# Optimization experiments

Hardware: AMD Instinct MI355X
Metric: run time of the kernel (lower is better)

Reference implementation:

```python
import jax, jax.numpy as jnp
import numpy as np

NUM_CLASSES = 80
IGNORE = 0.5
LABEL_SMOOTH = 0.0
MAX_GT = 20
C = 5 + NUM_CLASSES
SIZES = (13, 26, 52)
BS = 64
ANCHORS = jnp.array([
    [[0.0240, 0.0313], [0.0385, 0.0721], [0.0793, 0.0553]],
    [[0.0721, 0.1466], [0.1490, 0.1082], [0.1418, 0.2861]],
    [[0.2788, 0.2163], [0.3750, 0.4760], [0.8966, 0.7837]],
], dtype=jnp.float32)
ANCH_REV = ANCHORS[::-1]  # anchors[[2,1,0]] in the torch code


def bce(p, t):
    p = jnp.clip(p, 1e-7, 1.0 - 1e-7)
    return -t * jnp.log(p) - (1.0 - t) * jnp.log(1.0 - p)


def cal_iou(b1, b2):
    tl = jnp.maximum(b1[..., 0:2] - b1[..., 2:4] / 2, b2[..., 0:2] - b2[..., 2:4] / 2)
    br = jnp.minimum(b1[..., 0:2] + b1[..., 2:4] / 2, b2[..., 0:2] + b2[..., 2:4] / 2)
    wh = jnp.maximum(br - tl, 0.0)
    inter = wh[..., 0] * wh[..., 1]
    union = b1[..., 2] * b1[..., 3] + b2[..., 2] * b2[..., 3] - inter
    return inter / jnp.clip(union, 1e-6)


def _sample_loss(preds, tflat):
    # preds: [N, C] decoded (x,y,w,h,conf,cls...); tflat: [M, C] target grid flattened
    N = preds.shape[0]
    conf_t = tflat[:, 4]
    _, idx = jax.lax.top_k(conf_t, MAX_GT)      # gather up to MAX_GT GT slots
    gts = tflat[idx]                            # [K, C]
    gmask = gts[:, 4]                           # 1.0 for real GT, 0.0 for padding
    iou = cal_iou(gts[:, None, :4], preds[None, :, :4])  # [K, N]
    best = jnp.argmax(iou, axis=-1)             # [K]
    sel = preds[best]                           # [K, C]
    reg = jnp.sum((sel[:, :4] - gts[:, :4]) ** 2, axis=-1) * (2.0 - gts[:, 2] * gts[:, 3])
    loss_reg = jnp.sum(gmask * reg)
    tar_cls = gts[:, 5:] * (1.0 - LABEL_SMOOTH) + LABEL_SMOOTH / NUM_CLASSES
    loss_cls = jnp.sum(gmask[:, None] * bce(sel[:, 5:], tar_cls))
    # noobj mask: zero at best-matched preds (valid GTs only) and at high-IoU preds
    noobj = jnp.ones(N, preds.dtype).at[best].multiply(1.0 - gmask)
    maxiou = jnp.max(iou * gmask[:, None], axis=0)  # [N]
    noobj = noobj * (maxiou < IGNORE).astype(preds.dtype)
    loss_conf = jnp.sum(gmask * bce(sel[:, 4], 1.0)) + jnp.sum(noobj * bce(preds[:, 4], 0.0))
    return loss_reg + loss_conf + loss_cls


def _scale_loss(pred, tgt, l):
    bs, lsz = pred.shape[0], pred.shape[-1]
    p = pred.reshape(bs, 3, C, lsz, lsz).transpose(0, 1, 3, 4, 2)  # [bs,3,h,w,C]
    raw_w, raw_h = p[..., 2], p[..., 3]
    s = jax.nn.sigmoid(p)
    grid = jnp.arange(lsz, dtype=p.dtype)
    x = (grid[None, None, None, :] + s[..., 0]) / lsz
    y = (grid[None, None, :, None] + s[..., 1]) / lsz
    anch = ANCH_REV[l]  # [3,2]
    w = anch[:, 0][None, :, None, None] * jnp.exp(raw_w)
    h = anch[:, 1][None, :, None, None] * jnp.exp(raw_h)
    boxes = jnp.stack([x, y, w, h], axis=-1)
    preds = jnp.concatenate([boxes, s[..., 4:5], s[..., 5:]], axis=-1).reshape(bs, -1, C)
    tflat = tgt.reshape(bs, -1, C)
    return jnp.sum(jax.vmap(_sample_loss)(preds, tflat))


def setup_inputs() -> dict:
    key = jax.random.key(0)
    ks = jax.random.split(key, 6)
    inp = {}
    for i, lsz in enumerate(SIZES):
        inp['pred%d' % i] = jax.random.normal(ks[i], (BS, 3 * C, lsz, lsz), dtype=jnp.float32)
        M = 3 * lsz * lsz
        kb, ki, kc = jax.random.split(ks[3 + i], 3)
        xywh = jax.random.uniform(kb, (BS, MAX_GT, 4), minval=0.05, maxval=0.6, dtype=jnp.float32)
        cls_idx = jax.random.randint(kc, (BS, MAX_GT), 0, NUM_CLASSES)
        entry = jnp.concatenate([xywh, jnp.ones((BS, MAX_GT, 1), jnp.float32),
                                 jax.nn.one_hot(cls_idx, NUM_CLASSES, dtype=jnp.float32)], axis=-1)
        pos = jax.random.randint(ki, (BS, MAX_GT), 0, M)
        tflat = jnp.zeros((BS, M, C), jnp.float32).at[jnp.arange(BS)[:, None], pos].set(entry)
        inp['targets%d' % i] = tflat.reshape(BS, 3, lsz, lsz, C)
    return inp


def reference(pred0, pred1, pred2, targets0, targets1, targets2):
    return (_scale_loss(pred0, targets0, 0)
            + _scale_loss(pred1, targets1, 1)
            + _scale_loss(pred2, targets2, 2))
```

## Files before the change

### kernel.cpp

```cpp
#include <hip/hip_runtime.h>

#define CC 85
#define NC 80
#define MAXGT 20
#define BSZ 64
#define IGNORE_T 0.5f
#define CHUNK 1024

#define N0 507
#define N1 2028
#define N2 8112
#define R0 (BSZ*N0)
#define R1 (BSZ*N1)
#define R2 (BSZ*N2)
#define RTOT (R0+R1+R2)

#define POS_B   (192u*MAXGT*4u)
#define KEYS_B  (192u*MAXGT*8u)
#define NOOBJ_B (192u*4u)
#define HDR_B   (POS_B + KEYS_B + NOOBJ_B + 192u*4u)
#define BOX_B   ((unsigned)RTOT*16u)

__constant__ float d_anch[3][3][2] = {
  {{0.2788f,0.2163f},{0.375f,0.476f},{0.8966f,0.7837f}},
  {{0.0721f,0.1466f},{0.149f,0.1082f},{0.1418f,0.2861f}},
  {{0.024f,0.0313f},{0.0385f,0.0721f},{0.0793f,0.0553f}},
};
__constant__ int d_lsz[3] = {13,26,52};

__device__ __forceinline__ float sigmoidf(float x){ return 1.0f/(1.0f+__expf(-x)); }
__device__ __forceinline__ float bcef(float p, float t){
  p = fminf(fmaxf(p, 1e-7f), 1.0f-1e-7f);
  return -t*__logf(p) - (1.0f-t)*__logf(1.0f-p);
}
__device__ __forceinline__ float iouf(float gx,float gy,float gw,float gh,
                                      float px,float py,float pw,float ph){
  float tlx = fmaxf(gx-gw*0.5f, px-pw*0.5f);
  float tly = fmaxf(gy-gh*0.5f, py-ph*0.5f);
  float brx = fminf(gx+gw*0.5f, px+pw*0.5f);
  float bry = fminf(gy+gh*0.5f, py+ph*0.5f);
  float w = fmaxf(brx-tlx, 0.0f), h = fmaxf(bry-tly, 0.0f);
  float inter = w*h;
  float uni = gw*gh + pw*ph - inter;
  return inter / fmaxf(uni, 1e-6f);
}

template<int LSZ>
__device__ __forceinline__ void scanbox_one(const float* __restrict__ tgt,
                                            const float* __restrict__ pred,
                                            int rl, int s, int gofs,
                                            int* __restrict__ ws_pos,
                                            int* __restrict__ ws_cnt,
                                            float4* __restrict__ box4,
                                            float* __restrict__ confr){
  const int L2 = LSZ*LSZ, N = 3*L2;
  int b = rl / N;
  int n = rl - b*N;
  float c = tgt[(size_t)rl*CC + 4];
  if(c > 0.5f){
    int slot = s*BSZ + b;
    int i = atomicAdd(&ws_cnt[slot], 1);
    if(i < MAXGT) ws_pos[slot*MAXGT + i] = n;
  }
  int a = n / L2, rem = n - a*L2;
  int ii = rem / LSZ, jj = rem - ii*LSZ;
  const float* base = pred + (size_t)b*3*CC*L2 + (size_t)a*CC*L2 + rem;
  float q0 = base[0];
  float q1 = base[L2];
  float q2 = base[2*L2];
  float q3 = base[3*L2];
  float q4 = base[4*L2];
  const float inv = 1.0f/(float)LSZ;
  float px = ((float)jj + sigmoidf(q0))*inv;
  float py = ((float)ii + sigmoidf(q1))*inv;
  float pw = d_anch[s][a][0]*__expf(q2);
  float ph = d_anch[s][a][1]*__expf(q3);
  box4[gofs + rl] = make_float4(px,py,pw,ph);
  confr[gofs + rl] = q4;
}

__global__ __launch_bounds__(256)
void k_scanbox(const float* __restrict__ t0, const float* __restrict__ t1,
               const float* __restrict__ t2,
               const float* __restrict__ p0, const float* __restrict__ p1,
               const float* __restrict__ p2,
               int* __restrict__ ws_pos, int* __restrict__ ws_cnt,
               float4* __restrict__ box4, float* __restrict__ confr){
  int r = blockIdx.x*256 + threadIdx.x;
  if(r < R0)         scanbox_one<13>(t0, p0, r,       0, 0,     ws_pos, ws_cnt, box4, confr);
  else if(r < R0+R1) scanbox_one<26>(t1, p1, r-R0,    1, R0,    ws_pos, ws_cnt, box4, confr);
  else if(r < RTOT)  scanbox_one<52>(t2, p2, r-R0-R1, 2, R0+R1, ws_pos, ws_cnt, box4, confr);
}

__global__ __launch_bounds__(256, 2)
void k_iou(const float* __restrict__ t0, const float* __restrict__ t1,
           const float* __restrict__ t2,
           const float4* __restrict__ box4, const float* __restrict__ confr,
           const int* __restrict__ ws_pos, const int* __restrict__ ws_cnt,
           unsigned long long* __restrict__ ws_keys,
           float* __restrict__ ws_noobj){
  int s = blockIdx.z, b = blockIdx.y;
  int lsz = d_lsz[s], lsz2 = lsz*lsz, N = 3*lsz2;
  int n0 = blockIdx.x*CHUNK;
  if(n0 >= N) return;
  int slot = s*BSZ + b;
  int gofs = (s==0 ? 0 : (s==1 ? R0 : R0+R1)) + b*N;
  const float* tgt = (s==0 ? t0 : (s==1 ? t1 : t2)) + (size_t)b*N*CC;
  const float4* bx = box4 + gofs;
  const float*  cf = confr + gofs;
  int tid = threadIdx.x;
  __shared__ float gx[MAXGT], gy[MAXGT], gw[MAXGT], gh[MAXGT];
  __shared__ unsigned long long lkey[4][MAXGT];
  __shared__ float lnob[4];
  if(tid < MAXGT){
    int G = ws_cnt[slot];
    float x=0.f,y=0.f,w=0.f,h=0.f;
    if(tid < G){
      const float* r = tgt + (size_t)ws_pos[slot*MAXGT+tid]*CC;
      x=r[0]; y=r[1]; w=r[2]; h=r[3];
    }
    gx[tid]=x; gy[tid]=y; gw[tid]=w; gh[tid]=h;
  }
  __syncthreads();
  unsigned long long key[MAXGT];
  #pragma unroll
  for(int g=0; g<MAXGT; g++) key[g] = 0ull;
  float noobj = 0.0f;
  int nend = min(n0+CHUNK, N);
  for(int n=n0+tid; n<nend; n+=256){
    float4 B = bx[n];
    float q4 = cf[n];
    float maxiou = 0.0f;
    unsigned int ninv = ~(unsigned int)n;
    #pragma unroll
    for(int g=0; g<MAXGT; g++){
      float io = iouf(gx[g],gy[g],gw[g],gh[g], B.x,B.y,B.z,B.w);
      maxiou = fmaxf(maxiou, io);
      unsigned long long k = ((unsigned long long)__float_as_uint(io) << 32) | (unsigned long long)ninv;
      key[g] = (k > key[g]) ? k : key[g];
    }
    if(maxiou < IGNORE_T) noobj += bcef(sigmoidf(q4), 0.0f);
  }
  int wid = tid >> 6, lane = tid & 63;
  #pragma unroll
  for(int g=0; g<MAXGT; g++){
    unsigned long long k = key[g];
    for(int off=32; off>0; off>>=1){
      unsigned long long o = __shfl_down(k, off, 64);
      k = (o > k) ? o : k;
    }
    if(lane == 0) lkey[wid][g] = k;
  }
  for(int off=32; off>0; off>>=1) noobj += __shfl_down(noobj, off, 64);
  if(lane == 0) lnob[wid] = noobj;
  __syncthreads();
  if(tid < MAXGT){
    unsigned long long k0 = lkey[0][tid] > lkey[1][tid] ? lkey[0][tid] : lkey[1][tid];
    unsigned long long k1 = lkey[2][tid] > lkey[3][tid] ? lkey[2][tid] : lkey[3][tid];
    unsigned long long k  = k0 > k1 ? k0 : k1;
    atomicMax(&ws_keys[slot*MAXGT+tid], k);
  }
  if(tid == 0) atomicAdd(&ws_noobj[slot], lnob[0]+lnob[1]+lnob[2]+lnob[3]);
}

__global__ __launch_bounds__(256)
void k_final(const float* __restrict__ p0, const float* __restrict__ p1,
             const float* __restrict__ p2,
             const float* __restrict__ t0, const float* __restrict__ t1,
             const float* __restrict__ t2,
             const int* __restrict__ ws_pos, const int* __restrict__ ws_cnt,
             const unsigned long long* __restrict__ ws_keys,
             const float* __restrict__ ws_noobj,
             float* __restrict__ out){
  int b = blockIdx.x, s = blockIdx.y, z = blockIdx.z;
  int lsz = d_lsz[s], lsz2 = lsz*lsz, N = 3*lsz2;
  int slot = s*BSZ + b;
  const float* pred = (s==0 ? p0 : (s==1 ? p1 : p2)) + (size_t)b*3*CC*lsz2;
  const float* tgt  = (s==0 ? t0 : (s==1 ? t1 : t2)) + (size_t)b*N*CC;
  int tid = threadIdx.x;
  __shared__ int bn[MAXGT];
  __shared__ int gp[MAXGT];
  __shared__ float sx[MAXGT], sy[MAXGT], sw[MAXGT], sh[MAXGT];
  int G = ws_cnt[slot];
  if(tid < MAXGT){
    unsigned long long k = ws_keys[slot*MAXGT + tid];
    bn[tid] = (int)(~(unsigned int)(k & 0xffffffffull));
    float x=0.f,y=0.f,w=0.f,h=0.f; int p=0;
    if(tid < G){
      p = ws_pos[slot*MAXGT + tid];
      const float* r = tgt + (size_t)p*CC;
      x=r[0]; y=r[1]; w=r[2]; h=r[3];
    }
    gp[tid]=p; sx[tid]=x; sy[tid]=y; sw[tid]=w; sh[tid]=h;
  }
  __syncthreads();
  float loss = 0.0f;
  float inv = 1.0f/(float)lsz;
  if(z == 0 && tid < G){
    int n = bn[tid];
    int a = n/lsz2, rem = n - a*lsz2, i = rem/lsz, j = rem - i*lsz;
    const float* base = pred + (size_t)a*CC*lsz2 + rem;
    float q0 = base[0];
    float q1 = base[(size_t)lsz2];
    float q2 = base[2*(size_t)lsz2];
    float q3 = base[3*(size_t)lsz2];
    float q4 = base[4*(size_t)lsz2];
    float px = ((float)j + sigmoidf(q0))*inv;
    float py = ((float)i + sigmoidf(q1))*inv;
    float pw = d_anch[s][a][0]*__expf(q2);
    float ph = d_anch[s][a][1]*__expf(q3);
    float dx=px-sx[tid], dy=py-sy[tid], dw=pw-sw[tid], dh=ph-sh[tid];
    loss += (dx*dx + dy*dy + dw*dw + dh*dh) * (2.0f - sw[tid]*sh[tid]);
    loss += bcef(sigmoidf(q4), 1.0f);
    bool first = true;
    for(int g2=0; g2<tid; g2++) if(bn[g2]==n) first=false;
    if(first){
      float maxiou = 0.0f;
      for(int g2=0; g2<MAXGT; g2++)
        maxiou = fmaxf(maxiou, iouf(sx[g2],sy[g2],sw[g2],sh[g2], px,py,pw,ph));
      if(maxiou < IGNORE_T) loss -= bcef(sigmoidf(q4), 0.0f);
    }
  }
  for(int idx = z*256 + tid; idx < G*NC; idx += 1024){
    int g = idx/NC, c = idx - g*NC;
    int n = bn[g];
    int a = n/lsz2, rem = n - a*lsz2;
    float q = pred[(size_t)a*CC*lsz2 + (size_t)(5+c)*lsz2 + rem];
    float tcls = tgt[(size_t)gp[g]*CC + 5 + c];
    loss += bcef(sigmoidf(q), tcls);
  }
  if(z == 0 && tid == 0) loss += ws_noobj[slot];
  __shared__ float wsum[4];
  for(int off=32; off>0; off>>=1) loss += __shfl_down(loss, off, 64);
  if((tid & 63) == 0) wsum[tid>>6] = loss;
  __syncthreads();
  if(tid==0){
    float v = wsum[0]+wsum[1]+wsum[2]+wsum[3];
    if(v != 0.0f || z == 0) atomicAdd(out, v);
  }
}

extern "C" void kernel_launch(void* const* d_in, const int* in_sizes, int n_in,
                              void* d_out, int out_size, void* d_ws, size_t ws_size,
                              hipStream_t stream) {
  const float* p0 = (const float*)d_in[0];
  const float* t0 = (const float*)d_in[1];
  const float* p1 = (const float*)d_in[2];
  const float* t1 = (const float*)d_in[3];
  const float* p2 = (const float*)d_in[4];
  const float* t2 = (const float*)d_in[5];
  float* out = (float*)d_out;
  char* ws = (char*)d_ws;
  int*                ws_pos   = (int*)(ws);
  unsigned long long* ws_keys  = (unsigned long long*)(ws + POS_B);
  float*              ws_noobj = (float*)(ws + POS_B + KEYS_B);
  int*                ws_cnt   = (int*)(ws + POS_B + KEYS_B + NOOBJ_B);
  float4*             ws_box4  = (float4*)(ws + HDR_B);
  float*              ws_confr = (float*)(ws + HDR_B + BOX_B);

  hipMemsetAsync(ws, 0, HDR_B, stream);
  hipMemsetAsync(d_out, 0, sizeof(float), stream);

  k_scanbox<<<(RTOT+255)/256, 256, 0, stream>>>(t0,t1,t2, p0,p1,p2,
                                                ws_pos, ws_cnt, ws_box4, ws_confr);
  k_iou    <<<dim3(8,BSZ,3), 256, 0, stream>>>(t0,t1,t2, ws_box4, ws_confr,
                                               ws_pos, ws_cnt, ws_keys, ws_noobj);
  k_final  <<<dim3(BSZ,3,4), 256, 0, stream>>>(p0,p1,p2, t0,t1,t2,
                                               ws_pos, ws_cnt, ws_keys, ws_noobj, out);
}
```

Baseline: 412.8 us.

## Fuse scan, IoU and final loss into one block-per-sample kernel

Replaces the three-kernel pipeline (scan/box decode, chunked IoU, final loss) plus memsets with a single kernel that gives each (scale, batch) sample its own 512-thread block. That block finds the GT slots, decodes boxes in registers, computes IoU with GT corners and areas precomputed, and finishes the loss. A small second kernel then sums the per-slot results, which removes global atomics and the workspace round-trips for boxes. The risk is reduced parallelism: only 192 blocks run, and the 52x52 scale blocks each process 8112 cells serially, which may leave load imbalance and idle CUs.

New measurement: 421.0 us. Within noise of the previous version (+2.0%).

```diff
diff --git a/kernel.cpp b/kernel.cpp
--- a/kernel.cpp
+++ b/kernel.cpp
@@ -5,266 +5,225 @@
 #define MAXGT 20
 #define BSZ 64
 #define IGNORE_T 0.5f
-#define CHUNK 1024
-
-#define N0 507
-#define N1 2028
-#define N2 8112
-#define R0 (BSZ*N0)
-#define R1 (BSZ*N1)
-#define R2 (BSZ*N2)
-#define RTOT (R0+R1+R2)
-
-#define POS_B   (192u*MAXGT*4u)
-#define KEYS_B  (192u*MAXGT*8u)
-#define NOOBJ_B (192u*4u)
-#define HDR_B   (POS_B + KEYS_B + NOOBJ_B + 192u*4u)
-#define BOX_B   ((unsigned)RTOT*16u)
+#define BT 512
+#define NWAVE (BT/64)
 
 __constant__ float d_anch[3][3][2] = {
   {{0.2788f,0.2163f},{0.375f,0.476f},{0.8966f,0.7837f}},
   {{0.0721f,0.1466f},{0.149f,0.1082f},{0.1418f,0.2861f}},
   {{0.024f,0.0313f},{0.0385f,0.0721f},{0.0793f,0.0553f}},
 };
-__constant__ int d_lsz[3] = {13,26,52};
 
 __device__ __forceinline__ float sigmoidf(float x){ return 1.0f/(1.0f+__expf(-x)); }
 __device__ __forceinline__ float bcef(float p, float t){
   p = fminf(fmaxf(p, 1e-7f), 1.0f-1e-7f);
   return -t*__logf(p) - (1.0f-t)*__logf(1.0f-p);
 }
-__device__ __forceinline__ float iouf(float gx,float gy,float gw,float gh,
-                                      float px,float py,float pw,float ph){
-  float tlx = fmaxf(gx-gw*0.5f, px-pw*0.5f);
-  float tly = fmaxf(gy-gh*0.5f, py-ph*0.5f);
-  float brx = fminf(gx+gw*0.5f, px+pw*0.5f);
-  float bry = fminf(gy+gh*0.5f, py+ph*0.5f);
-  float w = fmaxf(brx-tlx, 0.0f), h = fmaxf(bry-tly, 0.0f);
-  float inter = w*h;
-  float uni = gw*gh + pw*ph - inter;
-  return inter / fmaxf(uni, 1e-6f);
-}
-
-template<int LSZ>
-__device__ __forceinline__ void scanbox_one(const float* __restrict__ tgt,
-                                            const float* __restrict__ pred,
-                                            int rl, int s, int gofs,
-                                            int* __restrict__ ws_pos,
-                                            int* __restrict__ ws_cnt,
-                                            float4* __restrict__ box4,
-                                            float* __restrict__ confr){
-  const int L2 = LSZ*LSZ, N = 3*L2;
-  int b = rl / N;
-  int n = rl - b*N;
-  float c = tgt[(size_t)rl*CC + 4];
-  if(c > 0.5f){
-    int slot = s*BSZ + b;
-    int i = atomicAdd(&ws_cnt[slot], 1);
-    if(i < MAXGT) ws_pos[slot*MAXGT + i] = n;
-  }
-  int a = n / L2, rem = n - a*L2;
-  int ii = rem / LSZ, jj = rem - ii*LSZ;
-  const float* base = pred + (size_t)b*3*CC*L2 + (size_t)a*CC*L2 + rem;
-  float q0 = base[0];
-  float q1 = base[L2];
-  float q2 = base[2*L2];
-  float q3 = base[3*L2];
-  float q4 = base[4*L2];
-  const float inv = 1.0f/(float)LSZ;
-  float px = ((float)jj + sigmoidf(q0))*inv;
-  float py = ((float)ii + sigmoidf(q1))*inv;
-  float pw = d_anch[s][a][0]*__expf(q2);
-  float ph = d_anch[s][a][1]*__expf(q3);
-  box4[gofs + rl] = make_float4(px,py,pw,ph);
-  confr[gofs + rl] = q4;
-}
-
-__global__ __launch_bounds__(256)
-void k_scanbox(const float* __restrict__ t0, const float* __restrict__ t1,
-               const float* __restrict__ t2,
-               const float* __restrict__ p0, const float* __restrict__ p1,
-               const float* __restrict__ p2,
-               int* __restrict__ ws_pos, int* __restrict__ ws_cnt,
-               float4* __restrict__ box4, float* __restrict__ confr){
-  int r = blockIdx.x*256 + threadIdx.x;
-  if(r < R0)         scanbox_one<13>(t0, p0, r,       0, 0,     ws_pos, ws_cnt, box4, confr);
-  else if(r < R0+R1) scanbox_one<26>(t1, p1, r-R0,    1, R0,    ws_pos, ws_cnt, box4, confr);
-  else if(r < RTOT)  scanbox_one<52>(t2, p2, r-R0-R1, 2, R0+R1, ws_pos, ws_cnt, box4, confr);
-}
-
-__global__ __launch_bounds__(256, 2)
-void k_iou(const float* __restrict__ t0, const float* __restrict__ t1,
-           const float* __restrict__ t2,
-           const float4* __restrict__ box4, const float* __restrict__ confr,
-           const int* __restrict__ ws_pos, const int* __restrict__ ws_cnt,
-           unsigned long long* __restrict__ ws_keys,
-           float* __restrict__ ws_noobj){
-  int s = blockIdx.z, b = blockIdx.y;
-  int lsz = d_lsz[s], lsz2 = lsz*lsz, N = 3*lsz2;
-  int n0 = blockIdx.x*CHUNK;
-  if(n0 >= N) return;
-  int slot = s*BSZ + b;
-  int gofs = (s==0 ? 0 : (s==1 ? R0 : R0+R1)) + b*N;
-  const float* tgt = (s==0 ? t0 : (s==1 ? t1 : t2)) + (size_t)b*N*CC;
-  const float4* bx = box4 + gofs;
-  const float*  cf = confr + gofs;
-  int tid = threadIdx.x;
-  __shared__ float gx[MAXGT], gy[MAXGT], gw[MAXGT], gh[MAXGT];
-  __shared__ unsigned long long lkey[4][MAXGT];
-  __shared__ float lnob[4];
-  if(tid < MAXGT){
-    int G = ws_cnt[slot];
+
+struct SlotSmem {
+  int cnt;
+  int pos[MAXGT];
+  int bn[MAXGT];
+  float gx[MAXGT], gy[MAXGT], gw[MAXGT], gh[MAXGT];
+  float4 tb[MAXGT];
+  float area[MAXGT];
+  unsigned long long lkey[NWAVE][MAXGT];
+  float lnob[NWAVE];
+  float lloss[NWAVE];
+};
+
+template<int LSZ, int S>
+__device__ __forceinline__ void slot_loss(const float* __restrict__ pred,
+                                          const float* __restrict__ tgt,
+                                          float* __restrict__ out_slot,
+                                          SlotSmem& sm)
+{
+  constexpr int L2 = LSZ*LSZ;
+  constexpr int N  = 3*L2;
+  const int tid = threadIdx.x;
+
+  if (tid == 0) sm.cnt = 0;
+  __syncthreads();
+  for (int n = tid; n < N; n += BT) {
+    if (tgt[(size_t)n*CC + 4] > 0.5f) {
+      int i = atomicAdd(&sm.cnt, 1);
+      if (i < MAXGT) sm.pos[i] = n;
+    }
+  }
+  __syncthreads();
+  const int G = min(sm.cnt, MAXGT);
+
+  if (tid < MAXGT) {
     float x=0.f,y=0.f,w=0.f,h=0.f;
-    if(tid < G){
-      const float* r = tgt + (size_t)ws_pos[slot*MAXGT+tid]*CC;
+    if (tid < G) {
+      const float* r = tgt + (size_t)sm.pos[tid]*CC;
       x=r[0]; y=r[1]; w=r[2]; h=r[3];
     }
-    gx[tid]=x; gy[tid]=y; gw[tid]=w; gh[tid]=h;
-  }
-  __syncthreads();
+    sm.gx[tid]=x; sm.gy[tid]=y; sm.gw[tid]=w; sm.gh[tid]=h;
+    sm.tb[tid] = make_float4(x-w*0.5f, y-h*0.5f, x+w*0.5f, y+h*0.5f);
+    sm.area[tid] = w*h;
+  }
+  __syncthreads();
+
   unsigned long long key[MAXGT];
   #pragma unroll
-  for(int g=0; g<MAXGT; g++) key[g] = 0ull;
+  for (int g=0; g<MAXGT; g++) key[g]=0ull;
   float noobj = 0.0f;
-  int nend = min(n0+CHUNK, N);
-  for(int n=n0+tid; n<nend; n+=256){
-    float4 B = bx[n];
-    float q4 = cf[n];
-    float maxiou = 0.0f;
-    unsigned int ninv = ~(unsigned int)n;
-    #pragma unroll
-    for(int g=0; g<MAXGT; g++){
-      float io = iouf(gx[g],gy[g],gw[g],gh[g], B.x,B.y,B.z,B.w);
-      maxiou = fmaxf(maxiou, io);
-      unsigned long long k = ((unsigned long long)__float_as_uint(io) << 32) | (unsigned long long)ninv;
-      key[g] = (k > key[g]) ? k : key[g];
-    }
-    if(maxiou < IGNORE_T) noobj += bcef(sigmoidf(q4), 0.0f);
-  }
-  int wid = tid >> 6, lane = tid & 63;
+  const float inv = 1.0f/(float)LSZ;
+
+  for (int base = 0; base < N; base += BT*4) {
+    float rx0[4],rx1[4],ry0[4],ry1[4],pa[4],q4v[4],maxi[4];
+    int nr[4];
+    #pragma unroll
+    for (int r=0;r<4;r++){
+      const int n = base + r*BT + tid;
+      nr[r]=n; maxi[r]=0.f;
+      if (n < N) {
+        const int a = n/L2, rem = n - a*L2;
+        const int ii = rem/LSZ, jj = rem - ii*LSZ;
+        const float* bp = pred + (size_t)a*CC*L2 + rem;
+        const float q0=bp[0], q1=bp[L2], q2=bp[2*L2], q3=bp[3*L2];
+        q4v[r]=bp[4*L2];
+        const float px = ((float)jj + sigmoidf(q0))*inv;
+        const float py = ((float)ii + sigmoidf(q1))*inv;
+        const float pw = d_anch[S][a][0]*__expf(q2);
+        const float ph = d_anch[S][a][1]*__expf(q3);
+        rx0[r]=px-pw*0.5f; rx1[r]=px+pw*0.5f;
+        ry0[r]=py-ph*0.5f; ry1[r]=py+ph*0.5f;
+        pa[r]=pw*ph;
+      } else {
+        rx0[r]=0.f; rx1[r]=0.f; ry0[r]=0.f; ry1[r]=0.f; pa[r]=0.f; q4v[r]=0.f;
+      }
+    }
+    #pragma unroll
+    for (int g=0; g<MAXGT; g++){
+      const float4 tb = sm.tb[g];
+      const float ga = sm.area[g];
+      #pragma unroll
+      for (int r=0;r<4;r++){
+        const float w = fmaxf(fminf(tb.z,rx1[r]) - fmaxf(tb.x,rx0[r]), 0.0f);
+        const float h = fmaxf(fminf(tb.w,ry1[r]) - fmaxf(tb.y,ry0[r]), 0.0f);
+        const float inter = w*h;
+        const float io = inter / fmaxf(ga + pa[r] - inter, 1e-6f);
+        maxi[r] = fmaxf(maxi[r], io);
+        const unsigned long long k =
+          ((unsigned long long)__float_as_uint(io)<<32) |
+          (unsigned long long)(~(unsigned)nr[r]);
+        if (k > key[g]) key[g] = k;
+      }
+    }
+    #pragma unroll
+    for (int r=0;r<4;r++)
+      if (nr[r] < N && maxi[r] < IGNORE_T) noobj += bcef(sigmoidf(q4v[r]), 0.0f);
+  }
+
+  const int wid = tid>>6, lane = tid&63;
   #pragma unroll
-  for(int g=0; g<MAXGT; g++){
+  for (int g=0; g<MAXGT; g++){
     unsigned long long k = key[g];
-    for(int off=32; off>0; off>>=1){
-      unsigned long long o = __shfl_down(k, off, 64);
-      k = (o > k) ? o : k;
-    }
-    if(lane == 0) lkey[wid][g] = k;
-  }
-  for(int off=32; off>0; off>>=1) noobj += __shfl_down(noobj, off, 64);
-  if(lane == 0) lnob[wid] = noobj;
-  __syncthreads();
-  if(tid < MAXGT){
-    unsigned long long k0 = lkey[0][tid] > lkey[1][tid] ? lkey[0][tid] : lkey[1][tid];
-    unsigned long long k1 = lkey[2][tid] > lkey[3][tid] ? lkey[2][tid] : lkey[3][tid];
-    unsigned long long k  = k0 > k1 ? k0 : k1;
-    atomicMax(&ws_keys[slot*MAXGT+tid], k);
-  }
-  if(tid == 0) atomicAdd(&ws_noobj[slot], lnob[0]+lnob[1]+lnob[2]+lnob[3]);
-}
-
-__global__ __launch_bounds__(256)
-void k_final(const float* __restrict__ p0, const float* __restrict__ p1,
-             const float* __restrict__ p2,
-             const float* __restrict__ t0, const float* __restrict__ t1,
-             const float* __restrict__ t2,
-             const int* __restrict__ ws_pos, const int* __restrict__ ws_cnt,
-             const unsigned long long* __restrict__ ws_keys,
-             const float* __restrict__ ws_noobj,
-             float* __restrict__ out){
-  int b = blockIdx.x, s = blockIdx.y, z = blockIdx.z;
-  int lsz = d_lsz[s], lsz2 = lsz*lsz, N = 3*lsz2;
-  int slot = s*BSZ + b;
-  const float* pred = (s==0 ? p0 : (s==1 ? p1 : p2)) + (size_t)b*3*CC*lsz2;
-  const float* tgt  = (s==0 ? t0 : (s==1 ? t1 : t2)) + (size_t)b*N*CC;
-  int tid = threadIdx.x;
-  __shared__ int bn[MAXGT];
-  __shared__ int gp[MAXGT];
-  __shared__ float sx[MAXGT], sy[MAXGT], sw[MAXGT], sh[MAXGT];
-  int G = ws_cnt[slot];
-  if(tid < MAXGT){
-    unsigned long long k = ws_keys[slot*MAXGT + tid];
-    bn[tid] = (int)(~(unsigned int)(k & 0xffffffffull));
-    float x=0.f,y=0.f,w=0.f,h=0.f; int p=0;
-    if(tid < G){
-      p = ws_pos[slot*MAXGT + tid];
-      const float* r = tgt + (size_t)p*CC;
-      x=r[0]; y=r[1]; w=r[2]; h=r[3];
-    }
-    gp[tid]=p; sx[tid]=x; sy[tid]=y; sw[tid]=w; sh[tid]=h;
-  }
-  __syncthreads();
+    for (int off=32; off>0; off>>=1){
+      const unsigned long long o = __shfl_down(k, off, 64);
+      if (o > k) k = o;
+    }
+    if (lane==0) sm.lkey[wid][g] = k;
+  }
+  for (int off=32; off>0; off>>=1) noobj += __shfl_down(noobj, off, 64);
+  if (lane==0) sm.lnob[wid] = noobj;
+  __syncthreads();
+  if (tid < MAXGT){
+    unsigned long long k = sm.lkey[0][tid];
+    #pragma unroll
+    for (int w=1; w<NWAVE; w++){ const unsigned long long o = sm.lkey[w][tid]; if (o>k) k=o; }
+    sm.bn[tid] = (int)(~(unsigned)(k & 0xffffffffull));
+  }
+  __syncthreads();
+
   float loss = 0.0f;
-  float inv = 1.0f/(float)lsz;
-  if(z == 0 && tid < G){
-    int n = bn[tid];
-    int a = n/lsz2, rem = n - a*lsz2, i = rem/lsz, j = rem - i*lsz;
-    const float* base = pred + (size_t)a*CC*lsz2 + rem;
-    float q0 = base[0];
-    float q1 = base[(size_t)lsz2];
-    float q2 = base[2*(size_t)lsz2];
-    float q3 = base[3*(size_t)lsz2];
-    float q4 = base[4*(size_t)lsz2];
-    float px = ((float)j + sigmoidf(q0))*inv;
-    float py = ((float)i + sigmoidf(q1))*inv;
-    float pw = d_anch[s][a][0]*__expf(q2);
-    float ph = d_anch[s][a][1]*__expf(q3);
-    float dx=px-sx[tid], dy=py-sy[tid], dw=pw-sw[tid], dh=ph-sh[tid];
-    loss += (dx*dx + dy*dy + dw*dw + dh*dh) * (2.0f - sw[tid]*sh[tid]);
+  if (tid < G){
+    const int n = sm.bn[tid];
+    const int a = n/L2, rem = n - a*L2, i = rem/LSZ, j = rem - i*LSZ;
+    const float* bp = pred + (size_t)a*CC*L2 + rem;
+    const float q0=bp[0], q1=bp[L2], q2=bp[2*L2], q3=bp[3*L2], q4=bp[4*L2];
+    const float px = ((float)j + sigmoidf(q0))*inv;
+    const float py = ((float)i + sigmoidf(q1))*inv;
+    const float pw = d_anch[S][a][0]*__expf(q2);
+    const float ph = d_anch[S][a][1]*__expf(q3);
+    const float dx=px-sm.gx[tid], dy=py-sm.gy[tid], dw=pw-sm.gw[tid], dh=ph-sm.gh[tid];
+    loss += (dx*dx+dy*dy+dw*dw+dh*dh)*(2.0f - sm.gw[tid]*sm.gh[tid]);
     loss += bcef(sigmoidf(q4), 1.0f);
     bool first = true;
-    for(int g2=0; g2<tid; g2++) if(bn[g2]==n) first=false;
-    if(first){
+    for (int g2=0; g2<tid; g2++) if (sm.bn[g2]==n) first=false;
+    if (first){
       float maxiou = 0.0f;
-      for(int g2=0; g2<MAXGT; g2++)
-        maxiou = fmaxf(maxiou, iouf(sx[g2],sy[g2],sw[g2],sh[g2], px,py,pw,ph));
-      if(maxiou < IGNORE_T) loss -= bcef(sigmoidf(q4), 0.0f);
-    }
-  }
-  for(int idx = z*256 + tid; idx < G*NC; idx += 1024){
-    int g = idx/NC, c = idx - g*NC;
-    int n = bn[g];
-    int a = n/lsz2, rem = n - a*lsz2;
-    float q = pred[(size_t)a*CC*lsz2 + (size_t)(5+c)*lsz2 + rem];
-    float tcls = tgt[(size_t)gp[g]*CC + 5 + c];
-    loss += bcef(sigmoidf(q), tcls);
-  }
-  if(z == 0 && tid == 0) loss += ws_noobj[slot];
-  __shared__ float wsum[4];
-  for(int off=32; off>0; off>>=1) loss += __shfl_down(loss, off, 64);
-  if((tid & 63) == 0) wsum[tid>>6] = loss;
-  __syncthreads();
-  if(tid==0){
-    float v = wsum[0]+wsum[1]+wsum[2]+wsum[3];
-    if(v != 0.0f || z == 0) atomicAdd(out, v);
-  }
+      const float bx0=px-pw*0.5f, bx1=px+pw*0.5f, by0=py-ph*0.5f, by1=py+ph*0.5f;
+      const float parea=pw*ph;
+      for (int g2=0; g2<MAXGT; g2++){
+        const float4 tb = sm.tb[g2];
+        const float w = fmaxf(fminf(tb.z,bx1) - fmaxf(tb.x,bx0), 0.0f);
+        const float h = fmaxf(fminf(tb.w,by1) - fmaxf(tb.y,by0), 0.0f);
+        const float inter = w*h;
+        maxiou = fmaxf(maxiou, inter / fmaxf(sm.area[g2]+parea-inter, 1e-6f));
+      }
+      if (maxiou < IGNORE_T) loss -= bcef(sigmoidf(q4), 0.0f);
+    }
+  }
+  for (int idx = tid; idx < G*NC; idx += BT){
+    const int g = idx/NC, c = idx - g*NC;
+    const int n = sm.bn[g];
+    const int a = n/L2, rem = n - a*L2;
+    const float q  = pred[(size_t)a*CC*L2 + (size_t)(5+c)*L2 + rem];
+    const float tc = tgt[(size_t)sm.pos[g]*CC + 5 + c];
+    loss += bcef(sigmoidf(q), tc);
+  }
+  for (int off=32; off>0; off>>=1) loss += __shfl_down(loss, off, 64);
+  if (lane==0) sm.lloss[wid] = loss;
+  __syncthreads();
+  if (tid==0){
+    float v = 0.f;
+    #pragma unroll
+    for (int w=0; w<NWAVE; w++) v += sm.lloss[w] + sm.lnob[w];
+    *out_slot = v;
+  }
+}
+
+__global__ __launch_bounds__(BT, 2)
+void k_fused(const float* __restrict__ p0, const float* __restrict__ t0,
+             const float* __restrict__ p1, const float* __restrict__ t1,
+             const float* __restrict__ p2, const float* __restrict__ t2,
+             float* __restrict__ slot_out)
+{
+  __shared__ SlotSmem sm;
+  const int b = blockIdx.x, s = blockIdx.y;
+  float* o = slot_out + s*BSZ + b;
+  if (s==0)      slot_loss<13,0>(p0 + (size_t)b*3*CC*13*13, t0 + (size_t)b*3*13*13*CC, o, sm);
+  else if (s==1) slot_loss<26,1>(p1 + (size_t)b*3*CC*26*26, t1 + (size_t)b*3*26*26*CC, o, sm);
+  else           slot_loss<52,2>(p2 + (size_t)b*3*CC*52*52, t2 + (size_t)b*3*52*52*CC, o, sm);
+}
+
+__global__ __launch_bounds__(256)
+void k_sum(const float* __restrict__ slot_in, float* __restrict__ out)
+{
+  const int tid = threadIdx.x;
+  float v = (tid < 3*BSZ) ? slot_in[tid] : 0.0f;
+  for (int off=32; off>0; off>>=1) v += __shfl_down(v, off, 64);
+  __shared__ float w[4];
+  if ((tid&63)==0) w[tid>>6] = v;
+  __syncthreads();
+  if (tid==0) out[0] = w[0]+w[1]+w[2]+w[3];
 }
 
 extern "C" void kernel_launch(void* const* d_in, const int* in_sizes, int n_in,
                               void* d_out, int out_size, void* d_ws, size_t ws_size,
-                              hipStream_t stream) {
+                              hipStream_t stream)
+{
   const float* p0 = (const float*)d_in[0];
   const float* t0 = (const float*)d_in[1];
   const float* p1 = (const float*)d_in[2];
   const float* t1 = (const float*)d_in[3];
   const float* p2 = (const float*)d_in[4];
   const float* t2 = (const float*)d_in[5];
-  float* out = (float*)d_out;
-  char* ws = (char*)d_ws;
-  int*                ws_pos   = (int*)(ws);
-  unsigned long long* ws_keys  = (unsigned long long*)(ws + POS_B);
-  float*              ws_noobj = (float*)(ws + POS_B + KEYS_B);
-  int*                ws_cnt   = (int*)(ws + POS_B + KEYS_B + NOOBJ_B);
-  float4*             ws_box4  = (float4*)(ws + HDR_B);
-  float*              ws_confr = (float*)(ws + HDR_B + BOX_B);
-
-  hipMemsetAsync(ws, 0, HDR_B, stream);
-  hipMemsetAsync(d_out, 0, sizeof(float), stream);
-
-  k_scanbox<<<(RTOT+255)/256, 256, 0, stream>>>(t0,t1,t2, p0,p1,p2,
-                                                ws_pos, ws_cnt, ws_box4, ws_confr);
-  k_iou    <<<dim3(8,BSZ,3), 256, 0, stream>>>(t0,t1,t2, ws_box4, ws_confr,
-                                               ws_pos, ws_cnt, ws_keys, ws_noobj);
-  k_final  <<<dim3(BSZ,3,4), 256, 0, stream>>>(p0,p1,p2, t0,t1,t2,
-                                               ws_pos, ws_cnt, ws_keys, ws_noobj, out);
-}
+  float* slot = (float*)d_ws;
+
+  k_fused<<<dim3(BSZ,3), BT, 0, stream>>>(p0,t0,p1,t1,p2,t2, slot);
+  k_sum  <<<1, 256, 0, stream>>>(slot, (float*)d_out);
+}
```
